# Kernel tuning notes

Measured on AMD Instinct MI355X. Metric: run time of the kernel, lower is better.

The kernel has to match this reference:

```python
import jax, jax.numpy as jnp
import numpy as np

B, S, M, D, F, H = 1, 2048, 512, 1024, 4096, 16
DH = D // H
W = 256  # Longformer half-window: query attends to keys within +/-W global positions


def layer_norm(x, g, b, eps=1e-5):
    mu = jnp.mean(x, axis=-1, keepdims=True)
    var = jnp.var(x, axis=-1, keepdims=True)
    return (x - mu) * jax.lax.rsqrt(var + eps) * g + b


def rel_sinusoid(dists, d_model):
    # Transformer-XL sinusoidal embedding of (possibly negative) relative distances
    inv_freq = 1.0 / (10000.0 ** (jnp.arange(0, d_model, 2, dtype=jnp.float32) / d_model))
    ang = dists[:, None].astype(jnp.float32) * inv_freq[None, :]
    return jnp.concatenate([jnp.sin(ang), jnp.cos(ang)], axis=-1)  # [nR, D]


def setup_inputs() -> dict:
    key = jax.random.key(0)
    ks = jax.random.split(key, 18)
    sc = D ** -0.5
    inp = {
        "x": jax.random.normal(ks[0], (B, S, D), jnp.float32),
        "mem": jax.random.normal(ks[1], (B, M, D), jnp.float32),
        "Wq": jax.random.normal(ks[2], (D, D), jnp.float32) * sc,
        "Wk": jax.random.normal(ks[3], (D, D), jnp.float32) * sc,
        "Wv": jax.random.normal(ks[4], (D, D), jnp.float32) * sc,
        "Wo": jax.random.normal(ks[5], (D, D), jnp.float32) * sc,
        "Wr": jax.random.normal(ks[6], (D, D), jnp.float32) * sc,
        "u": jax.random.normal(ks[7], (H, DH), jnp.float32) * 0.02,
        "v": jax.random.normal(ks[8], (H, DH), jnp.float32) * 0.02,
        "ln1_g": jnp.ones((D,), jnp.float32),
        "ln1_b": jnp.zeros((D,), jnp.float32),
        "W1": jax.random.normal(ks[9], (D, F), jnp.float32) * sc,
        "b1": jnp.zeros((F,), jnp.float32),
        "W2": jax.random.normal(ks[10], (F, D), jnp.float32) * (F ** -0.5),
        "b2": jnp.zeros((D,), jnp.float32),
        "ln2_g": jnp.ones((D,), jnp.float32),
        "ln2_b": jnp.zeros((D,), jnp.float32),
    }
    return inp


def reference(x, mem, Wq, Wk, Wv, Wo, Wr, u, v, ln1_g, ln1_b, W1, b1, W2, b2, ln2_g, ln2_b):
    L = M + S  # key/value length after prepending XL memory
    kv = jnp.concatenate([mem, x], axis=1)  # [B, L, D]
    q = (x @ Wq).reshape(B, S, H, DH)
    k = (kv @ Wk).reshape(B, L, H, DH)
    vv = (kv @ Wv).reshape(B, L, H, DH)

    # relative distances: global query pos = M+i, key pos = j -> dist = M+i-j in [-(S-1), M+S-1]
    dists = jnp.arange(-(S - 1), M + S)  # [nR]
    R = (rel_sinusoid(dists, D) @ Wr).reshape(-1, H, DH)  # [nR, H, DH]

    AC = jnp.einsum("bqhd,blhd->bhql", q + u, k)          # content term
    BD_all = jnp.einsum("bqhd,rhd->bhqr", q + v, R)        # position term per distance
    qi = jnp.arange(S)[:, None]
    kj = jnp.arange(L)[None, :]
    dist = M + qi - kj                                       # [S, L]
    idx = dist + (S - 1)
    BD = jnp.take_along_axis(BD_all, jnp.broadcast_to(idx[None, None], (B, H, S, L)), axis=-1)

    scores = (AC + BD) * (DH ** -0.5)
    band = jnp.abs(dist) <= W                                # sliding-window (banded) mask
    scores = jnp.where(band[None, None], scores, -1e30)
    attn = jax.nn.softmax(scores, axis=-1)
    o = jnp.einsum("bhql,blhd->bqhd", attn, vv).reshape(B, S, D) @ Wo

    h = layer_norm(x + o, ln1_g, ln1_b)                      # residual + LN (dropout: eval mode)
    f = jax.nn.gelu(h @ W1 + b1) @ W2 + b2                   # FFN
    return layer_norm(h + f, ln2_g, ln2_b)
```

## Files before the change

kernel.cpp:

```cpp
#include <hip/hip_runtime.h>
#include <hip/hip_bf16.h>
#include <cstdint>

#define S_ 2048
#define M_ 512
#define L_ 2560
#define D_ 1024
#define F_ 4096
#define H_ 16
#define DH_ 64
#define W_ 256
#define NR_ 513
#define NRP_ 640

typedef unsigned int uint32;
typedef __attribute__((ext_vector_type(8))) short bf16x8;
typedef __attribute__((ext_vector_type(4))) float f32x4;

__device__ __forceinline__ ushort f2bf(float f) {
  uint32 u = __builtin_bit_cast(uint32, f);
  u += 0x7FFFu + ((u >> 16) & 1u);
  return (ushort)(u >> 16);
}
__device__ __forceinline__ float bf2f(ushort s) {
  uint32 u = ((uint32)s) << 16;
  return __builtin_bit_cast(float, u);
}
__device__ __forceinline__ ushort4 pack4(float4 vf) {
  ushort4 r;
  r.x = f2bf(vf.x); r.y = f2bf(vf.y); r.z = f2bf(vf.z); r.w = f2bf(vf.w);
  return r;
}
__device__ __forceinline__ float gelu_tanh(float x) {
  float t = 0.7978845608028654f * x * (1.f + 0.044715f * x * x);
  float e = __expf(2.f * t);
  float th = 1.f - 2.f / (e + 1.f);
  return 0.5f * x * (1.f + th);
}

__device__ __forceinline__ void gld_lds16(const ushort* g, ushort* l) {
  __builtin_amdgcn_global_load_lds((const __attribute__((address_space(1))) void*)g,
                                   (__attribute__((address_space(3))) void*)l, 16, 0, 0);
}

__device__ __forceinline__ void tr_tile(const float* __restrict__ in, ushort* __restrict__ out,
                                        int R, int C, int c0, int r0, int tx, int ty,
                                        float (*tile)[33]) {
#pragma unroll
  for (int i = 0; i < 4; i++)
    tile[ty + i * 8][tx] = in[(size_t)(r0 + ty + i * 8) * C + c0 + tx];
  __syncthreads();
#pragma unroll
  for (int i = 0; i < 4; i++)
    out[(size_t)(c0 + ty + i * 8) * R + r0 + tx] = f2bf(tile[tx][ty + i * 8]);
}

__global__ __launch_bounds__(256)
void prep_kernel(const float* __restrict__ x, const float* __restrict__ mem,
                 const float* __restrict__ Wq, const float* __restrict__ Wk,
                 const float* __restrict__ Wv, const float* __restrict__ Wo,
                 const float* __restrict__ Wr, const float* __restrict__ W1,
                 const float* __restrict__ W2,
                 ushort* __restrict__ WqT, ushort* __restrict__ WkT,
                 ushort* __restrict__ WvT, ushort* __restrict__ WoT,
                 ushort* __restrict__ WrT, ushort* __restrict__ W1T,
                 ushort* __restrict__ W2T,
                 ushort* __restrict__ kvb, ushort* __restrict__ remb) {
  __shared__ float tile[32][33];
  const int bid = blockIdx.x;
  const int tid = threadIdx.x;
  const int tx = tid & 31, ty = tid >> 5;

  if (bid < 5120) {
    const int which = bid >> 10, idx = bid & 1023;
    const float* ins[5] = {Wq, Wk, Wv, Wo, Wr};
    ushort* outs[5] = {WqT, WkT, WvT, WoT, WrT};
    tr_tile(ins[which], outs[which], 1024, 1024, (idx & 31) * 32, (idx >> 5) * 32, tx, ty, tile);
  } else if (bid < 9216) {
    const int idx = bid - 5120;
    tr_tile(W1, W1T, 1024, 4096, (idx % 128) * 32, (idx / 128) * 32, tx, ty, tile);
  } else if (bid < 13312) {
    const int idx = bid - 9216;
    tr_tile(W2, W2T, 4096, 1024, (idx & 31) * 32, (idx >> 5) * 32, tx, ty, tile);
  } else if (bid < 15872) {
    const int k = (bid - 13312) * 256 + tid;
    const int l = k >> 8, c = k & 255;
    const float4* src = (l < M_) ? (const float4*)(mem + (size_t)l * D_)
                                 : (const float4*)(x + (size_t)(l - M_) * D_);
    ((ushort4*)kvb)[k] = pack4(src[c]);
  } else {
    const int idx = (bid - 15872) * 256 + tid;
    const int r = idx >> 9, f = idx & 511;
    if (r < NR_) {
      float invf = expf(-(float)f * (9.210340371976184f / 512.0f));
      float ang = (float)(r - W_) * invf;
      remb[(size_t)r * D_ + f] = f2bf(sinf(ang));
      remb[(size_t)r * D_ + 512 + f] = f2bf(cosf(ang));
    } else if (r < NRP_) {
      remb[(size_t)r * D_ + f] = 0;
      remb[(size_t)r * D_ + 512 + f] = 0;
    }
  }
}

template <int BM, int BN, int EPI, int SPLITK>
__device__ __forceinline__
void gemm_core(const ushort* __restrict__ A, const ushort* __restrict__ BT,
               void* __restrict__ Cout, void* __restrict__ Cout2,
               const float* __restrict__ bias, int Msz, int Nsz, int Ksz, int Kstride,
               int gx, int bid, int nwg, ushort* smem) {
  constexpr int PA = BM * 8 + 16;
  constexpr int PB = BN * 8 + 16;
  constexpr int MFR = BM / 32;
  constexpr int NFR = BN / 32;
  constexpr int NAI = (BM / 64) * 8;
  constexpr int NBI = (BN / 64) * 8;
  constexpr int NPW = (NAI + NBI) / 4;
  const int tid = threadIdx.x;
  const int wave = tid >> 6, lane = tid & 63;
  const int wr = wave >> 1, wc = wave & 1;

  const int q = nwg >> 3;
  const int swz = (bid & 7) * q + (bid >> 3);
  const int gy = Msz / BM;
  const int bx = swz % gx;
  const int rest = swz / gx;
  const int by = rest % gy;
  const int bz = rest / gy;

  const int brow = by * BM, bcol = bx * BN;
  const int koff = (SPLITK > 1) ? bz * Ksz : 0;

  ushort* As = smem;
  ushort* Bs = smem + 2 * 8 * PA;

  const ushort* gsrc[NPW]; int ldst[NPW];
#pragma unroll
  for (int i = 0; i < NPW; i++) {
    const int idx = i * 4 + wave;
    if (i < NAI / 4) {
      const int rowbase = (idx >> 3) * 64, kg = idx & 7;
      gsrc[i] = A + (size_t)(brow + rowbase + lane) * Kstride + koff + kg * 8;
      ldst[i] = kg * PA + rowbase * 8;
    } else {
      const int b = idx - NAI;
      const int rowbase = (b >> 3) * 64, kg = b & 7;
      gsrc[i] = BT + (size_t)(bcol + rowbase + lane) * Kstride + koff + kg * 8;
      ldst[i] = kg * PB + rowbase * 8;
    }
  }

  f32x4 acc[MFR][NFR] = {};
  const int kgf = lane >> 4, fr = lane & 15;
  const int nk = Ksz >> 6;

  auto stage = [&](int t, int buf) {
    const int ko = t * 64;
    ushort* ab = As + buf * 8 * PA;
    ushort* bb = Bs + buf * 8 * PB;
#pragma unroll
    for (int i = 0; i < NPW; i++) {
      ushort* base = (i < NAI / 4) ? ab : bb;
      gld_lds16(gsrc[i] + ko, base + ldst[i]);
    }
  };

  stage(0, 0);
  asm volatile("s_waitcnt vmcnt(0)" ::: "memory");
  __builtin_amdgcn_s_barrier();
  __builtin_amdgcn_sched_barrier(0);

  int cur = 0;
  for (int t = 0; t < nk; t++) {
    if (t + 1 < nk) stage(t + 1, cur ^ 1);
    ushort* ab = As + cur * 8 * PA;
    ushort* bb = Bs + cur * 8 * PB;
#pragma unroll
    for (int kk = 0; kk < 2; kk++) {
      bf16x8 af[MFR], bfv[NFR];
#pragma unroll
      for (int m = 0; m < MFR; m++)
        af[m] = *(const bf16x8*)(ab + (kk * 4 + kgf) * PA + (wr * (BM / 2) + m * 16 + fr) * 8);
#pragma unroll
      for (int n = 0; n < NFR; n++)
        bfv[n] = *(const bf16x8*)(bb + (kk * 4 + kgf) * PB + (wc * (BN / 2) + n * 16 + fr) * 8);
#pragma unroll
      for (int m = 0; m < MFR; m++)
#pragma unroll
        for (int n = 0; n < NFR; n++)
          acc[m][n] = __builtin_amdgcn_mfma_f32_16x16x32_bf16(af[m], bfv[n], acc[m][n], 0, 0, 0);
    }
    if (t + 1 < nk) {
      asm volatile("s_waitcnt vmcnt(0)" ::: "memory");
      __builtin_amdgcn_s_barrier();
      __builtin_amdgcn_sched_barrier(0);
    }
    cur ^= 1;
  }

  const int r4 = (lane >> 4) * 4;
  float* co = (float*)Cout;
  bool addb = (EPI == 3);
  if constexpr (SPLITK == 2) {
    if (bz == 1) { co = (float*)Cout2; addb = false; }
  }
#pragma unroll
  for (int m = 0; m < MFR; m++) {
#pragma unroll
    for (int n = 0; n < NFR; n++) {
      const int col = bcol + wc * (BN / 2) + n * 16 + fr;
#pragma unroll
      for (int r = 0; r < 4; r++) {
        const int row = brow + wr * (BM / 2) + m * 16 + r4 + r;
        float val = acc[m][n][r];
        size_t o = (size_t)row * Nsz + col;
        if constexpr (EPI == 0) ((ushort*)Cout)[o] = f2bf(val);
        else if constexpr (EPI == 2) ((ushort*)Cout)[o] = f2bf(gelu_tanh(val + bias[col]));
        else co[o] = addb ? val + bias[col] : val;
      }
    }
  }
}

template <int BM, int BN, int EPI, int SPLITK>
__global__ __launch_bounds__(256)
void gemm_kern(const ushort* __restrict__ A, const ushort* __restrict__ BT,
               void* __restrict__ Cout, void* __restrict__ Cout2,
               const float* __restrict__ bias, int Msz, int Nsz, int Ksz, int Kstride,
               int gx) {
  constexpr int PA = BM * 8 + 16, PB = BN * 8 + 16;
  __shared__ __align__(16) ushort smem[2 * 8 * (PA + PB)];
  gemm_core<BM, BN, EPI, SPLITK>(A, BT, Cout, Cout2, bias, Msz, Nsz, Ksz, Kstride,
                                 gx, blockIdx.x, gridDim.x, smem);
}

template <int EPI>
__device__ __forceinline__
void gemm8p2_core(const ushort* __restrict__ A, const ushort* __restrict__ BT,
                  void* __restrict__ Cout, void* __restrict__ Cout2,
                  const float* __restrict__ bias, int Msz, int Nsz, int Ksz, int Kstride,
                  int gx, int bid, int nwg, char* dyn) {
  const int tid = threadIdx.x;
  const int wave = tid >> 6, lane = tid & 63;
  const int wr = wave >> 2, wc = wave & 3;
  const int fr = lane & 15, gf = lane >> 4;
  const int sl = fr & 7;

  const int xcd = bid & 7, idx = bid >> 3;
  const int q = nwg >> 3, r8 = nwg & 7;
  const int swz = (xcd < r8 ? xcd * (q + 1) : r8 * (q + 1) + (xcd - r8) * q) + idx;
  const int bx = swz % gx, by = swz / gx;
  const int brow = by * 128, bcol = bx * 256;

  const int nt = Ksz >> 6;

  const int srow = tid >> 3;
  const int scol = ((tid & 7) ^ (srow & 7)) * 8;
  const ushort* Ab = A + (size_t)(brow + srow) * Kstride + scol;
  const ushort* Bb = BT + (size_t)(bcol + srow) * Kstride + scol;

  auto stageA = [&](int t, int qm) {
    gld_lds16(Ab + (size_t)(qm * 64) * Kstride + t * 64,
              (ushort*)(dyn + (t & 1) * 49152 + qm * 8192) + wave * 512);
  };
  auto stageB = [&](int t, int qn) {
#pragma unroll
    for (int j = 0; j < 2; j++)
      gld_lds16(Bb + (size_t)(qn * 128 + j * 64) * Kstride + t * 64,
                (ushort*)(dyn + (t & 1) * 49152 + 16384 + qn * 16384 + j * 8192) + wave * 512);
  };

  const int ar0 = (wr * 32 + fr) * 128;
  const int ar1 = (wr * 32 + 16 + fr) * 128;
  const int br0 = (wc * 32 + fr) * 128;
  const int br1 = (wc * 32 + 16 + fr) * 128;
  const int s0 = (gf ^ sl) * 16;
  const int s1 = ((4 + gf) ^ sl) * 16;

  f32x4 acc00[2][2] = {}, acc01[2][2] = {}, acc10[2][2] = {}, acc11[2][2] = {};

  stageA(0, 0); stageB(0, 0); stageB(0, 1); stageA(0, 1);
  stageA(1, 0); stageB(1, 0);
  asm volatile("s_waitcnt vmcnt(3)" ::: "memory");
  __builtin_amdgcn_s_barrier();
  __builtin_amdgcn_sched_barrier(0);

#define PH4(QM, QN, ACC, STAGES, WAITS)                                                 \
  {                                                                                     \
    const char* ab = dyn + cur * 49152 + (QM) * 8192;                                   \
    const char* bb = dyn + cur * 49152 + 16384 + (QN) * 16384;                          \
    bf16x8 a00 = *(const bf16x8*)(ab + ar0 + s0);                                       \
    bf16x8 a10 = *(const bf16x8*)(ab + ar1 + s0);                                       \
    bf16x8 a01 = *(const bf16x8*)(ab + ar0 + s1);                                       \
    bf16x8 a11 = *(const bf16x8*)(ab + ar1 + s1);                                       \
    bf16x8 b00 = *(const bf16x8*)(bb + br0 + s0);                                       \
    bf16x8 b10 = *(const bf16x8*)(bb + br1 + s0);                                       \
    bf16x8 b01 = *(const bf16x8*)(bb + br0 + s1);                                       \
    bf16x8 b11 = *(const bf16x8*)(bb + br1 + s1);                                       \
    STAGES;                                                                             \
    WAITS;                                                                              \
    __builtin_amdgcn_s_barrier();                                                       \
    asm volatile("s_waitcnt lgkmcnt(0)" ::: "memory");                                  \
    __builtin_amdgcn_sched_barrier(0);                                                  \
    __builtin_amdgcn_s_setprio(1);                                                      \
    ACC[0][0] = __builtin_amdgcn_mfma_f32_16x16x32_bf16(a00, b00, ACC[0][0], 0, 0, 0);  \
    ACC[0][1] = __builtin_amdgcn_mfma_f32_16x16x32_bf16(a00, b10, ACC[0][1], 0, 0, 0);  \
    ACC[1][0] = __builtin_amdgcn_mfma_f32_16x16x32_bf16(a10, b00, ACC[1][0], 0, 0, 0);  \
    ACC[1][1] = __builtin_amdgcn_mfma_f32_16x16x32_bf16(a10, b10, ACC[1][1], 0, 0, 0);  \
    ACC[0][0] = __builtin_amdgcn_mfma_f32_16x16x32_bf16(a01, b01, ACC[0][0], 0, 0, 0);  \
    ACC[0][1] = __builtin_amdgcn_mfma_f32_16x16x32_bf16(a01, b11, ACC[0][1], 0, 0, 0);  \
    ACC[1][0] = __builtin_amdgcn_mfma_f32_16x16x32_bf16(a11, b01, ACC[1][0], 0, 0, 0);  \
    ACC[1][1] = __builtin_amdgcn_mfma_f32_16x16x32_bf16(a11, b11, ACC[1][1], 0, 0, 0);  \
    __builtin_amdgcn_s_setprio(0);                                                      \
    __builtin_amdgcn_s_barrier();                                                       \
  }

  for (int t = 0; t < nt; t++) {
    const int cur = t & 1;
    PH4(0, 0, acc00, { if (t + 1 < nt) stageB(t + 1, 1); }, {});
    PH4(0, 1, acc01, { if (t + 1 < nt) stageA(t + 1, 1); }, {});
    PH4(1, 0, acc10, { if (t + 2 < nt) stageA(t + 2, 0); }, {});
    PH4(1, 1, acc11, { if (t + 2 < nt) stageB(t + 2, 0); },
        {
          if (t + 1 < nt) {
            if (t + 2 < nt) asm volatile("s_waitcnt vmcnt(3)" ::: "memory");
            else            asm volatile("s_waitcnt vmcnt(0)" ::: "memory");
          }
        });
  }
#undef PH4

  const int r4 = gf * 4;
  auto wrq = [&](const f32x4 (&ACC)[2][2], int QM, int QN) {
#pragma unroll
    for (int m = 0; m < 2; m++) {
#pragma unroll
      for (int n = 0; n < 2; n++) {
        const int col = bcol + QN * 128 + wc * 32 + n * 16 + fr;
        const int row0 = brow + QM * 64 + wr * 32 + m * 16 + r4;
        if constexpr (EPI == 5) {
          if (col < 1024) {
#pragma unroll
            for (int r = 0; r < 4; r++)
              ((ushort*)Cout)[(size_t)(row0 + r) * 1024 + col] = f2bf(ACC[m][n][r]);
          } else {
            ushort4 pk;
            pk.x = f2bf(ACC[m][n][0]); pk.y = f2bf(ACC[m][n][1]);
            pk.z = f2bf(ACC[m][n][2]); pk.w = f2bf(ACC[m][n][3]);
            *(ushort4*)((ushort*)Cout2 + (size_t)(col - 1024) * Msz + row0) = pk;
          }
        } else {
#pragma unroll
          for (int r = 0; r < 4; r++) {
            float val = ACC[m][n][r];
            size_t o = (size_t)(row0 + r) * Nsz + col;
            if constexpr (EPI == 2) ((ushort*)Cout)[o] = f2bf(gelu_tanh(val + bias[col]));
            else ((ushort*)Cout)[o] = f2bf(val);
          }
        }
      }
    }
  };
  wrq(acc00, 0, 0);
  wrq(acc01, 0, 1);
  wrq(acc10, 1, 0);
  wrq(acc11, 1, 1);
}

template <int EPI>
__global__ __launch_bounds__(512)
void gemm8p2_kern(const ushort* __restrict__ A, const ushort* __restrict__ BT,
                  void* __restrict__ Cout, void* __restrict__ Cout2,
                  const float* __restrict__ bias, int Msz, int Nsz, int Ksz, int Kstride,
                  int gx) {
  extern __shared__ __align__(16) char dyn[];
  gemm8p2_core<EPI>(A, BT, Cout, Cout2, bias, Msz, Nsz, Ksz, Kstride,
                    gx, blockIdx.x, gridDim.x, dyn);
}

__global__ __launch_bounds__(512)
void proj8p(const ushort* __restrict__ kvb, const ushort* __restrict__ WqT,
            const ushort* __restrict__ WkvT, const ushort* __restrict__ WrT,
            const ushort* __restrict__ remb,
            ushort* __restrict__ qb, ushort* __restrict__ kb,
            ushort* __restrict__ Vt, ushort* __restrict__ Rb) {
  extern __shared__ __align__(16) char dyn[];
  const int bid = blockIdx.x;
  if (bid < 64) {
    gemm8p2_core<0>(kvb + 512 * 1024, WqT, qb, nullptr, nullptr,
                    2048, 1024, 1024, 1024, 4, bid, 64, dyn);
  } else if (bid < 224) {
    gemm8p2_core<5>(kvb, WkvT, kb, Vt, nullptr,
                    2560, 2048, 1024, 1024, 8, bid - 64, 160, dyn);
  } else {
    gemm8p2_core<0>(remb, WrT, Rb, nullptr, nullptr,
                    640, 1024, 1024, 1024, 4, bid - 224, 20, dyn);
  }
}

__global__ __launch_bounds__(256)
void attn_mfma4(const ushort* __restrict__ qb, const ushort* __restrict__ kb,
                const ushort* __restrict__ Vt, const ushort* __restrict__ Rb,
                const float* __restrict__ ubias, const float* __restrict__ vbias,
                ushort* __restrict__ attb) {
  const int bid = blockIdx.x;
  const int swz = (bid & 7) * 64 + (bid >> 3);
  const int h = swz >> 5;
  const int i0 = (swz & 31) * 64;
  const int tid = threadIdx.x;
  const int wave = tid >> 6, lane = tid & 63;
  const int g = lane >> 4, fr = lane & 15;
  const int hD = h * DH_;

  __shared__ __align__(16) ushort ring[4][16][64];
  __shared__ __align__(16) ushort Pl[4][16][40];

  const int qi = i0 + wave * 16 + fr;
  bf16x8 afu[2], afv[2];
#pragma unroll
  for (int kst = 0; kst < 2; kst++) {
    const int dof = kst * 32 + g * 8;
    bf16x8 qv = *(const bf16x8*)(qb + (size_t)qi * D_ + hD + dof);
    const float* up = ubias + hD + dof;
    const float* vp = vbias + hD + dof;
    bf16x8 au, av;
#pragma unroll
    for (int j = 0; j < 8; j++) {
      float q = bf2f((ushort)qv[j]);
      au[j] = (short)f2bf(q + up[j]);
      av[j] = (short)f2bf(q + vp[j]);
    }
    afu[kst] = au; afv[kst] = av;
  }

  const int jb = 256 + i0;
  const int smax = 2303 - i0;
  const int sbase = wave * 16;

  auto produce = [&](int r0, bf16x8 rf0, bf16x8 rf1) {
    f32x4 acc = {};
    __builtin_amdgcn_s_setprio(1);
    acc = __builtin_amdgcn_mfma_f32_16x16x32_bf16(afv[0], rf0, acc, 0, 0, 0);
    acc = __builtin_amdgcn_mfma_f32_16x16x32_bf16(afv[1], rf1, acc, 0, 0, 0);
    __builtin_amdgcn_s_setprio(0);
#pragma unroll
    for (int rr = 0; rr < 4; rr++)
      ring[wave][g * 4 + rr][(r0 + fr) & 63] = f2bf(acc[rr]);
  };
  auto loadRrow = [&](int row, bf16x8* out0, bf16x8* out1) {
    const int rc = row < 0 ? 0 : row;
    *out0 = *(const bf16x8*)(Rb + (size_t)rc * D_ + hD + g * 8);
    *out1 = *(const bf16x8*)(Rb + (size_t)rc * D_ + hD + 32 + g * 8);
  };
  auto loadK = [&](int ch, bf16x8 (&kp)[2][2]) {
#pragma unroll
    for (int half = 0; half < 2; half++) {
      const int sa = sbase + ch * 32 + half * 16 + fr;
      const int jc = (jb + sa < L_ - 1) ? (jb + sa) : (L_ - 1);
      kp[half][0] = *(const bf16x8*)(kb + (size_t)jc * 1024 + hD + g * 8);
      kp[half][1] = *(const bf16x8*)(kb + (size_t)jc * 1024 + hD + 32 + g * 8);
    }
  };
  auto loadV = [&](int ch, bf16x8 (&vp)[4]) {
    int kc = jb + sbase + ch * 32 + g * 8;
    if (kc > L_ - 8) kc = L_ - 8;
#pragma unroll
    for (int n = 0; n < 4; n++)
      vp[n] = *(const bf16x8*)(Vt + (size_t)(hD + n * 16 + fr) * L_ + kc);
  };

#pragma unroll
  for (int t = 0; t < 3; t++) {
    const int r0 = 480 + t * 16;
    bf16x8 rf0, rf1;
    loadRrow(r0 + fr, &rf0, &rf1);
    produce(r0, rf0, rf1);
  }

  float m4[4], l4[4];
  f32x4 oacc[4] = {};
#pragma unroll
  for (int rr = 0; rr < 4; rr++) { m4[rr] = -1e30f; l4[rr] = 0.f; }

  bf16x8 kA[2][2], vA[4], kB[2][2], vB[4];
  bf16x8 rP0a, rP0b, rP1a, rP1b;
  loadK(0, kA); loadV(0, vA);

  auto body = [&](int ch, bf16x8 (&kU)[2][2], bf16x8 (&vU)[4],
                  bf16x8 (&kP)[2][2], bf16x8 (&vP)[4], bool first) -> bool {
    const int c0 = sbase + ch * 32;
    if (c0 > smax) return false;
    if (!first) {
      const int r0 = 480 - ch * 32;
      produce(r0, rP0a, rP0b);
      produce(r0 + 16, rP1a, rP1b);
    }
    if (ch < 16) {
      const int r0n = 480 - (ch + 1) * 32;
      loadRrow(r0n + fr, &rP0a, &rP0b);
      loadRrow(r0n + 16 + fr, &rP1a, &rP1b);
      loadK(ch + 1, kP);
      loadV(ch + 1, vP);
    }
    f32x4 sc[2];
#pragma unroll
    for (int half = 0; half < 2; half++) {
      f32x4 acc = {};
      __builtin_amdgcn_s_setprio(1);
      acc = __builtin_amdgcn_mfma_f32_16x16x32_bf16(afu[0], kU[half][0], acc, 0, 0, 0);
      acc = __builtin_amdgcn_mfma_f32_16x16x32_bf16(afu[1], kU[half][1], acc, 0, 0, 0);
      __builtin_amdgcn_s_setprio(0);
      const int rb2 = 512 + g * 4 - (ch * 32 + half * 16 + fr);
      const int sa = c0 + half * 16 + fr;
#pragma unroll
      for (int rr = 0; rr < 4; rr++) {
        const int r = rb2 + rr;
        const float bd = bf2f(ring[wave][g * 4 + rr][r & 63]);
        const bool valid = ((unsigned)r <= 512u) && (sa <= smax);
        sc[half][rr] = valid ? (acc[rr] + bd) * 0.125f : -1e30f;
      }
    }
    if (first) {
      f32x4 cm;
#pragma unroll
      for (int rr = 0; rr < 4; rr++) cm[rr] = fmaxf(sc[0][rr], sc[1][rr]);
#pragma unroll
      for (int off = 8; off; off >>= 1)
#pragma unroll
        for (int rr = 0; rr < 4; rr++) cm[rr] = fmaxf(cm[rr], __shfl_xor(cm[rr], off));
#pragma unroll
      for (int rr = 0; rr < 4; rr++) m4[rr] = cm[rr];
    } else {
      bool rise = false;
#pragma unroll
      for (int rr = 0; rr < 4; rr++)
        rise |= (fmaxf(sc[0][rr], sc[1][rr]) > m4[rr] + 8.f);
      if (__any(rise)) {
        f32x4 cm;
#pragma unroll
        for (int rr = 0; rr < 4; rr++) cm[rr] = fmaxf(sc[0][rr], sc[1][rr]);
#pragma unroll
        for (int off = 8; off; off >>= 1)
#pragma unroll
          for (int rr = 0; rr < 4; rr++) cm[rr] = fmaxf(cm[rr], __shfl_xor(cm[rr], off));
#pragma unroll
        for (int rr = 0; rr < 4; rr++) {
          const float nm = fmaxf(m4[rr], cm[rr]);
          const float esc = __expf(m4[rr] - nm);
          m4[rr] = nm;
          l4[rr] *= esc;
#pragma unroll
          for (int n = 0; n < 4; n++) oacc[n][rr] *= esc;
        }
      }
    }
    f32x4 pA, pB;
#pragma unroll
    for (int rr = 0; rr < 4; rr++) {
      pA[rr] = __expf(sc[0][rr] - m4[rr]);
      pB[rr] = __expf(sc[1][rr] - m4[rr]);
      l4[rr] += pA[rr] + pB[rr];
    }
#pragma unroll
    for (int rr = 0; rr < 4; rr++) {
      Pl[wave][g * 4 + rr][fr]      = f2bf(pA[rr]);
      Pl[wave][g * 4 + rr][16 + fr] = f2bf(pB[rr]);
    }
    bf16x8 pf = *(const bf16x8*)&Pl[wave][fr][g * 8];
    __builtin_amdgcn_s_setprio(1);
#pragma unroll
    for (int n = 0; n < 4; n++)
      oacc[n] = __builtin_amdgcn_mfma_f32_16x16x32_bf16(pf, vU[n], oacc[n], 0, 0, 0);
    __builtin_amdgcn_s_setprio(0);
    return true;
  };

  bool cont = body(0, kA, vA, kB, vB, true);
  for (int ch = 1; ch < 17 && cont; ch += 2) {
    cont = body(ch, kB, vB, kA, vA, false);
    if (!cont || ch + 1 >= 17) break;
    cont = body(ch + 1, kA, vA, kB, vB, false);
  }

#pragma unroll
  for (int off = 8; off; off >>= 1)
#pragma unroll
    for (int rr = 0; rr < 4; rr++) l4[rr] += __shfl_xor(l4[rr], off);
#pragma unroll
  for (int rr = 0; rr < 4; rr++) {
    const float inv = 1.f / l4[rr];
    const size_t rowo = (size_t)(i0 + sbase + g * 4 + rr) * D_ + hD;
#pragma unroll
    for (int n = 0; n < 4; n++)
      attb[rowo + n * 16 + fr] = f2bf(oacc[n][rr] * inv);
  }
}

__global__ __launch_bounds__(256)
void ln_kernel(const float* __restrict__ a, const float* __restrict__ b,
               const float* __restrict__ c,
               const float* __restrict__ gamma, const float* __restrict__ beta,
               float* __restrict__ outf, ushort* __restrict__ outb) {
  const int row = blockIdx.x;
  const int tid = threadIdx.x;
  const int wave = tid >> 6, lane = tid & 63;
  float4 va = ((const float4*)(a + (size_t)row * D_))[tid];
  float4 vb4 = ((const float4*)(b + (size_t)row * D_))[tid];
  float4 xv;
  xv.x = va.x + vb4.x; xv.y = va.y + vb4.y; xv.z = va.z + vb4.z; xv.w = va.w + vb4.w;
  if (c) {
    float4 vc = ((const float4*)(c + (size_t)row * D_))[tid];
    xv.x += vc.x; xv.y += vc.y; xv.z += vc.z; xv.w += vc.w;
  }
  float s = xv.x + xv.y + xv.z + xv.w;
  float q = xv.x * xv.x + xv.y * xv.y + xv.z * xv.z + xv.w * xv.w;
#pragma unroll
  for (int off = 32; off; off >>= 1) { s += __shfl_xor(s, off); q += __shfl_xor(q, off); }
  __shared__ float red[8];
  if (lane == 0) { red[wave * 2] = s; red[wave * 2 + 1] = q; }
  __syncthreads();
  float ts = red[0] + red[2] + red[4] + red[6];
  float tq = red[1] + red[3] + red[5] + red[7];
  float mu = ts * (1.f / D_);
  float var = tq * (1.f / D_) - mu * mu;
  float rs = rsqrtf(var + 1e-5f);
  float4 g4 = ((const float4*)gamma)[tid];
  float4 be4 = ((const float4*)beta)[tid];
  float4 y;
  y.x = (xv.x - mu) * rs * g4.x + be4.x;
  y.y = (xv.y - mu) * rs * g4.y + be4.y;
  y.z = (xv.z - mu) * rs * g4.z + be4.z;
  y.w = (xv.w - mu) * rs * g4.w + be4.w;
  ((float4*)(outf + (size_t)row * D_))[tid] = y;
  if (outb) ((ushort4*)(outb + (size_t)row * D_))[tid] = pack4(y);
}

extern "C" void kernel_launch(void* const* d_in, const int* in_sizes, int n_in,
                              void* d_out, int out_size, void* d_ws, size_t ws_size,
                              hipStream_t stream) {
  const float* x    = (const float*)d_in[0];
  const float* mem  = (const float*)d_in[1];
  const float* Wq   = (const float*)d_in[2];
  const float* Wk   = (const float*)d_in[3];
  const float* Wv   = (const float*)d_in[4];
  const float* Wo   = (const float*)d_in[5];
  const float* Wr   = (const float*)d_in[6];
  const float* u    = (const float*)d_in[7];
  const float* v    = (const float*)d_in[8];
  const float* ln1g = (const float*)d_in[9];
  const float* ln1b = (const float*)d_in[10];
  const float* W1   = (const float*)d_in[11];
  const float* b1   = (const float*)d_in[12];
  const float* W2   = (const float*)d_in[13];
  const float* b2   = (const float*)d_in[14];
  const float* ln2g = (const float*)d_in[15];
  const float* ln2b = (const float*)d_in[16];
  float* out = (float*)d_out;

  char* ws = (char*)d_ws;
  size_t off = 0;
  auto take = [&](size_t n) { char* p = ws + off; off += (n + 255) & ~(size_t)255; return p; };

  ushort* WqT = (ushort*)take(2097152);
  ushort* WkT = (ushort*)take(2097152);
  ushort* WvT = (ushort*)take(2097152);
  ushort* WoT = (ushort*)take(2097152);
  ushort* WrT = (ushort*)take(2097152);
  ushort* W1T = (ushort*)take(8388608);
  ushort* W2T = (ushort*)take(8388608);

  char* regA = take(8388608);
  ushort* kvb  = (ushort*)regA;
  ushort* remb = (ushort*)(regA + 5242880);
  float*  fbuf = (float*)regA;

  char* regB = take(20185088);
  ushort* qb   = (ushort*)regB;
  ushort* kb   = (ushort*)(regB + 4194304);
  ushort* Vt   = (ushort*)(regB + 9437184);
  ushort* Rb   = (ushort*)(regB + 14680064);
  ushort* attb = (ushort*)(regB + 15990784);
  float*  o2b  = (float*)regB;
  ushort* g    = (ushort*)regB;

  float*  o2 = (float*)take(8388608);
  float*  h  = (float*)take(8388608);
  ushort* hb = (ushort*)take(4194304);

  prep_kernel<<<17152, 256, 0, stream>>>(x, mem, Wq, Wk, Wv, Wo, Wr, W1, W2,
                                         WqT, WkT, WvT, WoT, WrT, W1T, W2T, kvb, remb);

  proj8p<<<244, 512, 98304, stream>>>(kvb, WqT, WkT, WrT, remb, qb, kb, Vt, Rb);

  attn_mfma4<<<512, 256, 0, stream>>>(qb, kb, Vt, Rb, u, v, attb);

  gemm_kern<64, 128, 1, 2><<<512, 256, 0, stream>>>(attb, WoT, o2, o2b, nullptr,
                                                    2048, 1024, 512, 1024, 8);
  ln_kernel<<<2048, 256, 0, stream>>>(x, o2, o2b, ln1g, ln1b, h, hb);

  gemm8p2_kern<2><<<256, 512, 98304, stream>>>(hb, W1T, g, nullptr, b1,
                                               2048, 4096, 1024, 1024, 16);

  gemm_kern<64, 128, 3, 2><<<512, 256, 0, stream>>>(g, W2T, fbuf, o2, b2,
                                                    2048, 1024, 2048, 4096, 8);
  ln_kernel<<<2048, 256, 0, stream>>>(h, fbuf, o2, ln2g, ln2b, out, nullptr);
}
```

Baseline: 208.9 us.

## Use 128x256 8-wave GEMM with split-K for output projection and FFN2

Removes the generic 64x128 4-wave GEMM and routes the Wo projection (split-K 2) and the W2 FFN GEMM (split-K 4) through the larger 128x256 tile kernel. It adds a fp32 split-K epilogue to that kernel, with extra partial-output pointers. The LayerNorm kernel now sums up to five inputs to reduce the partials. The extra partials live in the transposed-weight scratch buffers WqT and W1T, which are no longer needed at that point. The aim is better MFMA efficiency and data reuse per block. The cost is fewer blocks for Wo, only 128, and more fp32 partial traffic into LayerNorm; reusing WqT as an 8MB buffer depends on how the workspace is laid out.

```diff
diff --git a/kernel.cpp b/kernel.cpp
--- a/kernel.cpp
+++ b/kernel.cpp
@@ -103,141 +103,11 @@
   }
 }
 
-template <int BM, int BN, int EPI, int SPLITK>
-__device__ __forceinline__
-void gemm_core(const ushort* __restrict__ A, const ushort* __restrict__ BT,
-               void* __restrict__ Cout, void* __restrict__ Cout2,
-               const float* __restrict__ bias, int Msz, int Nsz, int Ksz, int Kstride,
-               int gx, int bid, int nwg, ushort* smem) {
-  constexpr int PA = BM * 8 + 16;
-  constexpr int PB = BN * 8 + 16;
-  constexpr int MFR = BM / 32;
-  constexpr int NFR = BN / 32;
-  constexpr int NAI = (BM / 64) * 8;
-  constexpr int NBI = (BN / 64) * 8;
-  constexpr int NPW = (NAI + NBI) / 4;
-  const int tid = threadIdx.x;
-  const int wave = tid >> 6, lane = tid & 63;
-  const int wr = wave >> 1, wc = wave & 1;
-
-  const int q = nwg >> 3;
-  const int swz = (bid & 7) * q + (bid >> 3);
-  const int gy = Msz / BM;
-  const int bx = swz % gx;
-  const int rest = swz / gx;
-  const int by = rest % gy;
-  const int bz = rest / gy;
-
-  const int brow = by * BM, bcol = bx * BN;
-  const int koff = (SPLITK > 1) ? bz * Ksz : 0;
-
-  ushort* As = smem;
-  ushort* Bs = smem + 2 * 8 * PA;
-
-  const ushort* gsrc[NPW]; int ldst[NPW];
-#pragma unroll
-  for (int i = 0; i < NPW; i++) {
-    const int idx = i * 4 + wave;
-    if (i < NAI / 4) {
-      const int rowbase = (idx >> 3) * 64, kg = idx & 7;
-      gsrc[i] = A + (size_t)(brow + rowbase + lane) * Kstride + koff + kg * 8;
-      ldst[i] = kg * PA + rowbase * 8;
-    } else {
-      const int b = idx - NAI;
-      const int rowbase = (b >> 3) * 64, kg = b & 7;
-      gsrc[i] = BT + (size_t)(bcol + rowbase + lane) * Kstride + koff + kg * 8;
-      ldst[i] = kg * PB + rowbase * 8;
-    }
-  }
-
-  f32x4 acc[MFR][NFR] = {};
-  const int kgf = lane >> 4, fr = lane & 15;
-  const int nk = Ksz >> 6;
-
-  auto stage = [&](int t, int buf) {
-    const int ko = t * 64;
-    ushort* ab = As + buf * 8 * PA;
-    ushort* bb = Bs + buf * 8 * PB;
-#pragma unroll
-    for (int i = 0; i < NPW; i++) {
-      ushort* base = (i < NAI / 4) ? ab : bb;
-      gld_lds16(gsrc[i] + ko, base + ldst[i]);
-    }
-  };
-
-  stage(0, 0);
-  asm volatile("s_waitcnt vmcnt(0)" ::: "memory");
-  __builtin_amdgcn_s_barrier();
-  __builtin_amdgcn_sched_barrier(0);
-
-  int cur = 0;
-  for (int t = 0; t < nk; t++) {
-    if (t + 1 < nk) stage(t + 1, cur ^ 1);
-    ushort* ab = As + cur * 8 * PA;
-    ushort* bb = Bs + cur * 8 * PB;
-#pragma unroll
-    for (int kk = 0; kk < 2; kk++) {
-      bf16x8 af[MFR], bfv[NFR];
-#pragma unroll
-      for (int m = 0; m < MFR; m++)
-        af[m] = *(const bf16x8*)(ab + (kk * 4 + kgf) * PA + (wr * (BM / 2) + m * 16 + fr) * 8);
-#pragma unroll
-      for (int n = 0; n < NFR; n++)
-        bfv[n] = *(const bf16x8*)(bb + (kk * 4 + kgf) * PB + (wc * (BN / 2) + n * 16 + fr) * 8);
-#pragma unroll
-      for (int m = 0; m < MFR; m++)
-#pragma unroll
-        for (int n = 0; n < NFR; n++)
-          acc[m][n] = __builtin_amdgcn_mfma_f32_16x16x32_bf16(af[m], bfv[n], acc[m][n], 0, 0, 0);
-    }
-    if (t + 1 < nk) {
-      asm volatile("s_waitcnt vmcnt(0)" ::: "memory");
-      __builtin_amdgcn_s_barrier();
-      __builtin_amdgcn_sched_barrier(0);
-    }
-    cur ^= 1;
-  }
-
-  const int r4 = (lane >> 4) * 4;
-  float* co = (float*)Cout;
-  bool addb = (EPI == 3);
-  if constexpr (SPLITK == 2) {
-    if (bz == 1) { co = (float*)Cout2; addb = false; }
-  }
-#pragma unroll
-  for (int m = 0; m < MFR; m++) {
-#pragma unroll
-    for (int n = 0; n < NFR; n++) {
-      const int col = bcol + wc * (BN / 2) + n * 16 + fr;
-#pragma unroll
-      for (int r = 0; r < 4; r++) {
-        const int row = brow + wr * (BM / 2) + m * 16 + r4 + r;
-        float val = acc[m][n][r];
-        size_t o = (size_t)row * Nsz + col;
-        if constexpr (EPI == 0) ((ushort*)Cout)[o] = f2bf(val);
-        else if constexpr (EPI == 2) ((ushort*)Cout)[o] = f2bf(gelu_tanh(val + bias[col]));
-        else co[o] = addb ? val + bias[col] : val;
-      }
-    }
-  }
-}
-
-template <int BM, int BN, int EPI, int SPLITK>
-__global__ __launch_bounds__(256)
-void gemm_kern(const ushort* __restrict__ A, const ushort* __restrict__ BT,
-               void* __restrict__ Cout, void* __restrict__ Cout2,
-               const float* __restrict__ bias, int Msz, int Nsz, int Ksz, int Kstride,
-               int gx) {
-  constexpr int PA = BM * 8 + 16, PB = BN * 8 + 16;
-  __shared__ __align__(16) ushort smem[2 * 8 * (PA + PB)];
-  gemm_core<BM, BN, EPI, SPLITK>(A, BT, Cout, Cout2, bias, Msz, Nsz, Ksz, Kstride,
-                                 gx, blockIdx.x, gridDim.x, smem);
-}
-
-template <int EPI>
+template <int EPI, int SPLITK>
 __device__ __forceinline__
 void gemm8p2_core(const ushort* __restrict__ A, const ushort* __restrict__ BT,
                   void* __restrict__ Cout, void* __restrict__ Cout2,
+                  void* __restrict__ Cout3, void* __restrict__ Cout4,
                   const float* __restrict__ bias, int Msz, int Nsz, int Ksz, int Kstride,
                   int gx, int bid, int nwg, char* dyn) {
   const int tid = threadIdx.x;
@@ -249,15 +119,20 @@
   const int xcd = bid & 7, idx = bid >> 3;
   const int q = nwg >> 3, r8 = nwg & 7;
   const int swz = (xcd < r8 ? xcd * (q + 1) : r8 * (q + 1) + (xcd - r8) * q) + idx;
-  const int bx = swz % gx, by = swz / gx;
+  const int gy = Msz / 128;
+  const int bx = swz % gx;
+  const int rest = swz / gx;
+  const int by = rest % gy;
+  const int bz = rest / gy;
   const int brow = by * 128, bcol = bx * 256;
+  const int koff = (SPLITK > 1) ? bz * Ksz : 0;
 
   const int nt = Ksz >> 6;
 
   const int srow = tid >> 3;
   const int scol = ((tid & 7) ^ (srow & 7)) * 8;
-  const ushort* Ab = A + (size_t)(brow + srow) * Kstride + scol;
-  const ushort* Bb = BT + (size_t)(bcol + srow) * Kstride + scol;
+  const ushort* Ab = A + (size_t)(brow + srow) * Kstride + koff + scol;
+  const ushort* Bb = BT + (size_t)(bcol + srow) * Kstride + koff + scol;
 
   auto stageA = [&](int t, int qm) {
     gld_lds16(Ab + (size_t)(qm * 64) * Kstride + t * 64,
@@ -331,6 +206,15 @@
 #undef PH4
 
   const int r4 = gf * 4;
+  float* co = (float*)Cout;
+  bool addb = (EPI == 3);
+  if constexpr (SPLITK >= 2) {
+    if (bz == 1) { co = (float*)Cout2; addb = false; }
+  }
+  if constexpr (SPLITK == 4) {
+    if (bz == 2) { co = (float*)Cout3; addb = false; }
+    if (bz == 3) { co = (float*)Cout4; addb = false; }
+  }
   auto wrq = [&](const f32x4 (&ACC)[2][2], int QM, int QN) {
 #pragma unroll
     for (int m = 0; m < 2; m++) {
@@ -349,7 +233,7 @@
             pk.z = f2bf(ACC[m][n][2]); pk.w = f2bf(ACC[m][n][3]);
             *(ushort4*)((ushort*)Cout2 + (size_t)(col - 1024) * Msz + row0) = pk;
           }
-        } else {
+        } else if constexpr (EPI == 0 || EPI == 2) {
 #pragma unroll
           for (int r = 0; r < 4; r++) {
             float val = ACC[m][n][r];
@@ -357,6 +241,12 @@
             if constexpr (EPI == 2) ((ushort*)Cout)[o] = f2bf(gelu_tanh(val + bias[col]));
             else ((ushort*)Cout)[o] = f2bf(val);
           }
+        } else {
+#pragma unroll
+          for (int r = 0; r < 4; r++) {
+            float val = ACC[m][n][r];
+            co[(size_t)(row0 + r) * Nsz + col] = addb ? val + bias[col] : val;
+          }
         }
       }
     }
@@ -367,15 +257,16 @@
   wrq(acc11, 1, 1);
 }
 
-template <int EPI>
+template <int EPI, int SPLITK>
 __global__ __launch_bounds__(512)
 void gemm8p2_kern(const ushort* __restrict__ A, const ushort* __restrict__ BT,
                   void* __restrict__ Cout, void* __restrict__ Cout2,
+                  void* __restrict__ Cout3, void* __restrict__ Cout4,
                   const float* __restrict__ bias, int Msz, int Nsz, int Ksz, int Kstride,
                   int gx) {
   extern __shared__ __align__(16) char dyn[];
-  gemm8p2_core<EPI>(A, BT, Cout, Cout2, bias, Msz, Nsz, Ksz, Kstride,
-                    gx, blockIdx.x, gridDim.x, dyn);
+  gemm8p2_core<EPI, SPLITK>(A, BT, Cout, Cout2, Cout3, Cout4, bias,
+                            Msz, Nsz, Ksz, Kstride, gx, blockIdx.x, gridDim.x, dyn);
 }
 
 __global__ __launch_bounds__(512)
@@ -387,14 +278,14 @@
   extern __shared__ __align__(16) char dyn[];
   const int bid = blockIdx.x;
   if (bid < 64) {
-    gemm8p2_core<0>(kvb + 512 * 1024, WqT, qb, nullptr, nullptr,
-                    2048, 1024, 1024, 1024, 4, bid, 64, dyn);
+    gemm8p2_core<0, 1>(kvb + 512 * 1024, WqT, qb, nullptr, nullptr, nullptr, nullptr,
+                       2048, 1024, 1024, 1024, 4, bid, 64, dyn);
   } else if (bid < 224) {
-    gemm8p2_core<5>(kvb, WkvT, kb, Vt, nullptr,
-                    2560, 2048, 1024, 1024, 8, bid - 64, 160, dyn);
+    gemm8p2_core<5, 1>(kvb, WkvT, kb, Vt, nullptr, nullptr, nullptr,
+                       2560, 2048, 1024, 1024, 8, bid - 64, 160, dyn);
   } else {
-    gemm8p2_core<0>(remb, WrT, Rb, nullptr, nullptr,
-                    640, 1024, 1024, 1024, 4, bid - 224, 20, dyn);
+    gemm8p2_core<0, 1>(remb, WrT, Rb, nullptr, nullptr, nullptr, nullptr,
+                       640, 1024, 1024, 1024, 4, bid - 224, 20, dyn);
   }
 }
 
@@ -598,7 +489,8 @@
 
 __global__ __launch_bounds__(256)
 void ln_kernel(const float* __restrict__ a, const float* __restrict__ b,
-               const float* __restrict__ c,
+               const float* __restrict__ c, const float* __restrict__ d,
+               const float* __restrict__ e,
                const float* __restrict__ gamma, const float* __restrict__ beta,
                float* __restrict__ outf, ushort* __restrict__ outb) {
   const int row = blockIdx.x;
@@ -611,6 +503,14 @@
   if (c) {
     float4 vc = ((const float4*)(c + (size_t)row * D_))[tid];
     xv.x += vc.x; xv.y += vc.y; xv.z += vc.z; xv.w += vc.w;
+  }
+  if (d) {
+    float4 vd = ((const float4*)(d + (size_t)row * D_))[tid];
+    xv.x += vd.x; xv.y += vd.y; xv.z += vd.z; xv.w += vd.w;
+  }
+  if (e) {
+    float4 ve = ((const float4*)(e + (size_t)row * D_))[tid];
+    xv.x += ve.x; xv.y += ve.y; xv.z += ve.z; xv.w += ve.w;
   }
   float s = xv.x + xv.y + xv.z + xv.w;
   float q = xv.x * xv.x + xv.y * xv.y + xv.z * xv.z + xv.w * xv.w;
@@ -687,6 +587,9 @@
   float*  h  = (float*)take(8388608);
   ushort* hb = (ushort*)take(4194304);
 
+  float* p2 = (float*)WqT;
+  float* p3 = (float*)W1T;
+
   prep_kernel<<<17152, 256, 0, stream>>>(x, mem, Wq, Wk, Wv, Wo, Wr, W1, W2,
                                          WqT, WkT, WvT, WoT, WrT, W1T, W2T, kvb, remb);
 
@@ -694,14 +597,14 @@
 
   attn_mfma4<<<512, 256, 0, stream>>>(qb, kb, Vt, Rb, u, v, attb);
 
-  gemm_kern<64, 128, 1, 2><<<512, 256, 0, stream>>>(attb, WoT, o2, o2b, nullptr,
-                                                    2048, 1024, 512, 1024, 8);
-  ln_kernel<<<2048, 256, 0, stream>>>(x, o2, o2b, ln1g, ln1b, h, hb);
-
-  gemm8p2_kern<2><<<256, 512, 98304, stream>>>(hb, W1T, g, nullptr, b1,
-                                               2048, 4096, 1024, 1024, 16);
-
-  gemm_kern<64, 128, 3, 2><<<512, 256, 0, stream>>>(g, W2T, fbuf, o2, b2,
-                                                    2048, 1024, 2048, 4096, 8);
-  ln_kernel<<<2048, 256, 0, stream>>>(h, fbuf, o2, ln2g, ln2b, out, nullptr);
-}
+  gemm8p2_kern<1, 2><<<128, 512, 98304, stream>>>(attb, WoT, o2, o2b, nullptr, nullptr,
+                                                  nullptr, 2048, 1024, 512, 1024, 4);
+  ln_kernel<<<2048, 256, 0, stream>>>(x, o2, o2b, nullptr, nullptr, ln1g, ln1b, h, hb);
+
+  gemm8p2_kern<2, 1><<<256, 512, 98304, stream>>>(hb, W1T, g, nullptr, nullptr, nullptr,
+                                                  b1, 2048, 4096, 1024, 1024, 16);
+
+  gemm8p2_kern<3, 4><<<256, 512, 98304, stream>>>(g, W2T, fbuf, o2, p2, p3,
+                                                  b2, 2048, 1024, 1024, 4096, 4);
+  ln_kernel<<<2048, 256, 0, stream>>>(h, fbuf, o2, p2, p3, ln2g, ln2b, out, nullptr);
+}
```

Result: faster. 189.3 us (-9.4%).
